# Kernel tuning notes

Measured on AMD Instinct MI355X. Metric: run time of the kernel, lower is better.

## Reference

```python
import jax, jax.numpy as jnp
import numpy as np

B, T, C = 4, 1024, 512      # batch, seq_len, n_attn
H, TT, D = 1, 1024, 16      # n_head (forced to 1 by kv.view), ctx_len, head_size


def setup_inputs() -> dict:
    key = jax.random.key(0)
    ks = jax.random.split(key, 13)
    s = 0.02
    return {
        "x": jax.random.normal(ks[0], (B, T, C), jnp.float32),
        "time_w": 1.0 + 0.1 * jax.random.normal(ks[1], (H, TT), jnp.float32),
        "time_alpha": 1.0 + 0.1 * jax.random.normal(ks[2], (H, 1, TT), jnp.float32),
        "time_beta": 1.0 + 0.1 * jax.random.normal(ks[3], (H, TT, 1), jnp.float32),
        "time_gamma": 1.0 + 0.1 * jax.random.normal(ks[4], (TT, 1), jnp.float32),
        "Wk": s * jax.random.normal(ks[5], (D, C), jnp.float32),
        "bk": jnp.zeros((D,), jnp.float32),
        "Wv": s * jax.random.normal(ks[6], (D, C), jnp.float32),
        "bv": jnp.zeros((D,), jnp.float32),
        "Wr": s * jax.random.normal(ks[7], (D, C), jnp.float32),
        "br": jnp.zeros((D,), jnp.float32),
        "Wo": s * jax.random.normal(ks[8], (64, D), jnp.float32),
        "bo": jnp.zeros((64,), jnp.float32),
    }


def reference(x, time_w, time_alpha, time_beta, time_gamma,
              Wk, bk, Wv, bv, Wr, br, Wo, bo):
    Tq = x.shape[1]
    # --- Toeplitz decay-matrix build (pad / tile / reshape trick) ---
    w = jnp.pad(time_w, ((0, 0), (0, TT)))                    # [H, 2TT]
    w = jnp.tile(w, (1, TT))[:, :-TT]                         # [H, 2TT*TT - TT]
    w = w.reshape(-1, TT, 2 * TT - 1)[:, :, TT - 1:]          # [H, TT, TT]
    w = w[:, :Tq, :Tq] * time_alpha[:, :, :Tq] * time_beta[:, :Tq, :]  # [H, T, T]
    # --- time shift on first half of channels (ZeroPad2d((0,0,1,-1))) ---
    half = x.shape[-1] // 2
    xs = jnp.pad(x[:, :, :half], ((0, 0), (1, 0), (0, 0)))[:, :-1]   # shift right by 1
    xx = jnp.concatenate([xs, x[:, :, half:]], axis=-1)              # [B, T, C]
    # --- k / v / r projections ---
    k = jnp.exp(jnp.clip(xx @ Wk.T + bk, -60.0, 30.0))        # [B, T, D]
    v = xx @ Wv.T + bv                                        # [B, T, D]
    r = xx @ Wr.T + br                                        # [B, T, D]
    sum_k = jnp.cumsum(k, axis=1)                             # [B, T, D]
    kv = k * v                                                # [B, T, D]
    # torch: kv.view(B,T,1,D).transpose(1,2) -> [B,1,T,D]; einsum 'htu,bthd->bhud'
    # broadcasts w's h=1 against kv's time axis and kv's t=1 against w's t axis:
    #   wkv[b,h,u,d] = (sum_t w[0,t,u]) * kv[b,h(time),d]
    w_sum = jnp.sum(w, axis=1)[0]                             # [T] over u
    wkv_full = w_sum[None, None, :, None] * kv[:, :, None, :] # [B, T, T, D]
    wkv = jnp.mean(wkv_full, axis=1)                          # mean over h -> [B, T, D]
    rwkv = r * wkv / (sum_k + 1e-8)                           # [B, T, D]
    out = (rwkv @ Wo.T + bo) * time_gamma[:Tq, :]             # [B, T, 64]
    return out
```

## Files before the change

kernel.cpp:

```cpp
#include <hip/hip_runtime.h>
#include <hip/hip_bf16.h>

typedef __hip_bfloat16 bf16;


__device__ __forceinline__ float ldf(const void* p, int f, long idx) {
    if (f == 0) return ((const float*)p)[idx];
    if (f == 1) {
        unsigned int u = ((unsigned int)((const unsigned short*)p)[idx]) << 16;
        float r; __builtin_memcpy(&r, &u, 4); return r;
    }
    return 0.f;
}

__global__ __launch_bounds__(64) void sniff_kernel(
    const void* p0, const void* p1, const void* p2, const void* p3,
    const void* p4, const void* p5, const void* p6, const void* p7,
    const void* p8, const void* p9, const void* p10, const void* p11,
    const void* p12,
    int n0, int n1, int n2, int n3, int n4, int n5, int n6, int n7,
    int n8, int n9, int n10, int n11, int n12,
    int* flags)
{
    const void* ps[13] = {p0,p1,p2,p3,p4,p5,p6,p7,p8,p9,p10,p11,p12};
    int ns[13] = {n0,n1,n2,n3,n4,n5,n6,n7,n8,n9,n10,n11,n12};
    int i = threadIdx.x;
    if (i < 13) {
        const unsigned short* u = (const unsigned short*)ps[i];
        int n16 = ns[i] < 64 ? ns[i] : 64;
        bool allzero = true;
        for (int j = 0; j < n16; ++j) if (u[j] != 0) { allzero = false; break; }
        int flag;
        if (allzero) flag = 2;
        else {
            int npair = n16 / 2;
            bool all_bf = true;
            for (int j = 0; j < npair; ++j) {
                unsigned short lo = u[2 * j], hi = u[2 * j + 1];
                int elo = (lo >> 7) & 0xFF, ehi = (hi >> 7) & 0xFF;
                bool lo_ok = (elo >= 64 && elo <= 190) || lo == 0;
                bool hi_ok = (ehi >= 64 && ehi <= 190) || hi == 0;
                if (!(lo_ok && hi_ok)) { all_bf = false; break; }
            }
            flag = all_bf ? 1 : 0;
        }
        flags[i] = flag;
    }
    __syncthreads();
    if (i == 0) {
        int any16 = 0;
        for (int j = 0; j < 13; ++j) if (flags[j] == 1) any16 = 1;
        flags[13] = any16;
    }
}

__global__ __launch_bounds__(256) void prep_kernel(
    const void* Wk, const void* bk, const void* Wv, const void* bv,
    const void* Wr, const void* br, const void* Wo, const void* bo,
    const void* gamma, const int* __restrict__ flg,
    float* __restrict__ WT4, float* __restrict__ biasWS,
    float* __restrict__ WoF, float* __restrict__ boF, float* __restrict__ gammaF)
{
    int idx = blockIdx.x * 256 + threadIdx.x;
    if (idx < 32768) {
        int q = idx >> 8, rem = idx & 255;
        int o = rem >> 2, c = q * 4 + (rem & 3);
        float val = 0.f;
        if (o < 16)      val = ldf(Wk, flg[5], (long)o * 512 + c);
        else if (o < 32) val = ldf(Wv, flg[7], (long)(o - 16) * 512 + c);
        else if (o < 48) val = ldf(Wr, flg[9], (long)(o - 32) * 512 + c);
        WT4[idx] = val;
    } else if (idx < 33792) {
        int i = idx - 32768;
        WoF[i] = ldf(Wo, flg[11], i);
    } else if (idx < 34816) {
        int i = idx - 33792;
        gammaF[i] = ldf(gamma, flg[4], i);
    } else if (idx < 34880) {
        int i = idx - 34816;
        boF[i] = ldf(bo, flg[12], i);
    } else if (idx < 34944) {
        int i = idx - 34880;
        float bb = 0.f;
        if (i < 16)      bb = ldf(bk, flg[6], i);
        else if (i < 32) bb = ldf(bv, flg[8], i - 16);
        else if (i < 48) bb = ldf(br, flg[10], i - 32);
        biasWS[i] = bb;
    }
}

__global__ __launch_bounds__(256) void proj_kernel(
    const void* __restrict__ x, const float* __restrict__ WT4,
    const float* __restrict__ biasWS, const int* __restrict__ flg,
    float* __restrict__ k_ws, float* __restrict__ v_ws, float* __restrict__ r_ws)
{
    __shared__ float xs[16 * 512];
    __shared__ float red[4 * 16 * 64];
    int tid = threadIdx.x;
    int row0 = blockIdx.x * 16;
    int b = row0 >> 10;
    int lt0 = row0 & 1023;
    int fx = flg[0];

    if (fx == 1) {
        const unsigned short* xp = (const unsigned short*)x;
        #pragma unroll
        for (int j = 0; j < 8; ++j) {
            int v = tid + 256 * j;
            int el = v * 4;
            int r = el >> 9, c = el & 511;
            int lt = lt0 + r - ((c < 256) ? 1 : 0);
            float4 f;
            if (lt < 0) f = make_float4(0.f, 0.f, 0.f, 0.f);
            else {
                const unsigned short* sp = xp + ((long)(b * 1024 + lt) * 512 + c);
                unsigned int u0 = ((unsigned int)sp[0]) << 16;
                unsigned int u1 = ((unsigned int)sp[1]) << 16;
                unsigned int u2 = ((unsigned int)sp[2]) << 16;
                unsigned int u3 = ((unsigned int)sp[3]) << 16;
                __builtin_memcpy(&f.x, &u0, 4); __builtin_memcpy(&f.y, &u1, 4);
                __builtin_memcpy(&f.z, &u2, 4); __builtin_memcpy(&f.w, &u3, 4);
            }
            reinterpret_cast<float4*>(xs)[v] = f;
        }
    } else {
        const float* xp = (const float*)x;
        #pragma unroll
        for (int j = 0; j < 8; ++j) {
            int v = tid + 256 * j;
            int el = v * 4;
            int r = el >> 9, c = el & 511;
            int lt = lt0 + r - ((c < 256) ? 1 : 0);
            float4 f;
            if (lt < 0) f = make_float4(0.f, 0.f, 0.f, 0.f);
            else f = *reinterpret_cast<const float4*>(xp + ((long)(b * 1024 + lt) * 512 + c));
            reinterpret_cast<float4*>(xs)[v] = f;
        }
    }
    __syncthreads();

    int o = tid & 63, cc = tid >> 6;
    const float4* xs4 = reinterpret_cast<const float4*>(xs);
    const float4* W4 = reinterpret_cast<const float4*>(WT4);
    float acc[16];
    #pragma unroll
    for (int r = 0; r < 16; ++r) acc[r] = 0.f;
    int qbase = cc * 32;
    for (int q = 0; q < 32; ++q) {
        int cq = qbase + q;
        float4 w4 = W4[cq * 64 + o];
        #pragma unroll
        for (int r = 0; r < 16; ++r) {
            float4 x4 = xs4[r * 128 + cq];
            acc[r] += x4.x * w4.x + x4.y * w4.y + x4.z * w4.z + x4.w * w4.w;
        }
    }
    #pragma unroll
    for (int r = 0; r < 16; ++r)
        red[(cc * 16 + r) * 64 + o] = acc[r];
    __syncthreads();

    #pragma unroll
    for (int it = 0; it < 4; ++it) {
        int idx = tid + 256 * it;
        int o2 = idx & 63, r2 = idx >> 6;
        float s = red[(0 * 16 + r2) * 64 + o2] + red[(1 * 16 + r2) * 64 + o2]
                + red[(2 * 16 + r2) * 64 + o2] + red[(3 * 16 + r2) * 64 + o2]
                + biasWS[o2];
        if (o2 < 48) {
            int d = o2 & 15;
            long a = (long)(lt0 + r2) * 64 + b * 16 + d;
            if (o2 < 16)      k_ws[a] = expf(fminf(fmaxf(s, -60.f), 30.f));
            else if (o2 < 32) v_ws[a] = s;
            else              r_ws[a] = s;
        }
    }
}

__global__ __launch_bounds__(64) void wsum_kernel(
    const void* __restrict__ tw, const void* __restrict__ alpha,
    const void* __restrict__ beta, const int* __restrict__ flg,
    float* __restrict__ w_sum)
{
    int ftw = flg[1], fal = flg[2], fbe = flg[3];
    int u = blockIdx.x;
    int lane = threadIdx.x;
    __shared__ float red[64];
    float acc = 0.f;
    int n = 1024 - u;
    for (int s = lane; s < n; s += 64)
        acc += ldf(tw, ftw, 1023 - s) * ldf(beta, fbe, u + s);
    red[lane] = acc;
    __syncthreads();
    for (int off = 32; off > 0; off >>= 1) {
        if (lane < off) red[lane] += red[lane + off];
        __syncthreads();
    }
    if (lane == 0) w_sum[u] = red[0] * ldf(alpha, fal, u);
}

__global__ __launch_bounds__(64) void scanA_kernel(
    const float* __restrict__ k_ws, const float* __restrict__ v_ws,
    float* __restrict__ segsum, float* __restrict__ segkv)
{
    int seg = blockIdx.x, bd = threadIdx.x;
    float part = 0.f, kvp = 0.f;
    for (int i = 0; i < 64; ++i) {
        long a = (long)(seg * 64 + i) * 64 + bd;
        float kk = k_ws[a];
        part += kk;
        kvp += kk * v_ws[a];
    }
    segsum[seg * 64 + bd] = part;
    segkv[seg * 64 + bd] = kvp;
}

__global__ __launch_bounds__(64) void scanB_kernel(
    float* k_ws, const float* __restrict__ segsum,
    const float* __restrict__ segkv, float* __restrict__ kvmean)
{
    int seg = blockIdx.x, bd = threadIdx.x;
    float run = 0.f;
    for (int s = 0; s < seg; ++s) run += segsum[s * 64 + bd];
    for (int i = 0; i < 64; ++i) {
        long a = (long)(seg * 64 + i) * 64 + bd;
        run += k_ws[a];
        k_ws[a] = run;
    }
    if (seg == 0) {
        float kvt = 0.f;
        for (int s = 0; s < 16; ++s) kvt += segkv[s * 64 + bd];
        kvmean[bd] = kvt * (1.0f / 1024.0f);
    }
}

__global__ __launch_bounds__(256) void out_kernel(
    const float* __restrict__ r_ws, const float* __restrict__ cumk,
    const float* __restrict__ kvmean, const float* __restrict__ w_sum,
    const float* __restrict__ WoF, const float* __restrict__ boF,
    const float* __restrict__ gammaF, const int* __restrict__ flg,
    void* __restrict__ out)
{
    int tid = threadIdx.x;
    int rl = tid >> 6, o = tid & 63;
    int row = blockIdx.x * 4 + rl;
    int b = row >> 10, t = row & 1023;
    __shared__ float rw[4][16];
    if (o < 16) {
        long a = (long)t * 64 + b * 16 + o;
        rw[rl][o] = r_ws[a] * w_sum[t] * kvmean[b * 16 + o] / (cumk[a] + 1e-8f);
    }
    __syncthreads();
    float acc = boF[o];
    const float4* W4 = reinterpret_cast<const float4*>(WoF + o * 16);
    #pragma unroll
    for (int j = 0; j < 4; ++j) {
        float4 w = W4[j];
        acc += rw[rl][4 * j + 0] * w.x + rw[rl][4 * j + 1] * w.y +
               rw[rl][4 * j + 2] * w.z + rw[rl][4 * j + 3] * w.w;
    }
    float val = acc * gammaF[t];
    if (flg[13]) ((bf16*)out)[(long)row * 64 + o] = __float2bfloat16(val);
    else         ((float*)out)[(long)row * 64 + o] = val;
}

extern "C" void kernel_launch(void* const* d_in, const int* in_sizes, int n_in,
                              void* d_out, int out_size, void* d_ws, size_t ws_size,
                              hipStream_t stream) {
    const void* x     = d_in[0];
    const void* tw    = d_in[1];
    const void* alpha = d_in[2];
    const void* beta  = d_in[3];
    const void* gamma = d_in[4];
    const void* Wk    = d_in[5];
    const void* bk    = d_in[6];
    const void* Wv    = d_in[7];
    const void* bv    = d_in[8];
    const void* Wr    = d_in[9];
    const void* br    = d_in[10];
    const void* Wo    = d_in[11];
    const void* bo    = d_in[12];

    float* ws     = (float*)d_ws;
    float* k_ws   = ws;
    float* v_ws   = ws + 65536;
    float* r_ws   = ws + 131072;
    float* WT4    = ws + 196608;
    float* biasWS = ws + 229376;
    float* WoF    = ws + 229440;
    float* boF    = ws + 230464;
    float* gammaF = ws + 230528;
    float* kvmean = ws + 231552;
    float* w_sum  = ws + 231616;
    float* segsum = ws + 232640;
    float* segkv  = ws + 233664;
    int*   flags  = (int*)(ws + 234688);

    sniff_kernel<<<1, 64, 0, stream>>>(
        x, tw, alpha, beta, gamma, Wk, bk, Wv, bv, Wr, br, Wo, bo,
        in_sizes[0], in_sizes[1], in_sizes[2], in_sizes[3], in_sizes[4],
        in_sizes[5], in_sizes[6], in_sizes[7], in_sizes[8], in_sizes[9],
        in_sizes[10], in_sizes[11], in_sizes[12],
        flags);
    prep_kernel<<<137, 256, 0, stream>>>(Wk, bk, Wv, bv, Wr, br, Wo, bo,
                                         gamma, flags,
                                         WT4, biasWS, WoF, boF, gammaF);
    proj_kernel<<<256, 256, 0, stream>>>(x, WT4, biasWS, flags,
                                         k_ws, v_ws, r_ws);
    wsum_kernel<<<1024, 64, 0, stream>>>(tw, alpha, beta, flags, w_sum);
    scanA_kernel<<<16, 64, 0, stream>>>(k_ws, v_ws, segsum, segkv);
    scanB_kernel<<<16, 64, 0, stream>>>(k_ws, segsum, segkv, kvmean);
    out_kernel<<<1024, 256, 0, stream>>>(r_ws, k_ws, kvmean, w_sum,
                                         WoF, boF, gammaF, flags, (void*)d_out);
}
```

Before: 123.6 us.

## Fuse sniff, prep and wsum kernels; retile projection to 8 rows per block

Merges the dtype-sniff, weight-prep and w_sum reduction kernels into one 1024-block setup kernel. Each block redoes the sniff locally into shared memory instead of relying on a separate launch, which removes two kernel launches and their serialization. The projection kernel now handles 8 rows per block over 512 blocks. Each thread computes 4 outputs across a 16-way channel split, so the kernel gets more parallelism and better register reuse of x. The cost is a larger 16-way shared-memory reduction and redundant sniff reads in every setup block.

Result: faster. 114.3 us (-7.5%).

```diff
diff --git a/kernel.cpp b/kernel.cpp
--- a/kernel.cpp
+++ b/kernel.cpp
@@ -13,80 +13,89 @@
     return 0.f;
 }
 
-__global__ __launch_bounds__(64) void sniff_kernel(
-    const void* p0, const void* p1, const void* p2, const void* p3,
-    const void* p4, const void* p5, const void* p6, const void* p7,
-    const void* p8, const void* p9, const void* p10, const void* p11,
-    const void* p12,
+__device__ __forceinline__ int sniff_one(const unsigned short* u, int els) {
+    int n16 = els < 64 ? els : 64;
+    bool allzero = true;
+    for (int j = 0; j < n16; ++j) if (u[j] != 0) { allzero = false; break; }
+    if (allzero) return 2;
+    int npair = n16 / 2;
+    for (int j = 0; j < npair; ++j) {
+        unsigned short lo = u[2 * j], hi = u[2 * j + 1];
+        int elo = (lo >> 7) & 0xFF, ehi = (hi >> 7) & 0xFF;
+        bool lo_ok = (elo >= 64 && elo <= 190) || lo == 0;
+        bool hi_ok = (ehi >= 64 && ehi <= 190) || hi == 0;
+        if (!(lo_ok && hi_ok)) return 0;
+    }
+    return 1;
+}
+
+__global__ __launch_bounds__(256) void setup_kernel(
+    const void* x, const void* tw, const void* alpha, const void* beta,
+    const void* gamma, const void* Wk, const void* bk, const void* Wv,
+    const void* bv, const void* Wr, const void* br, const void* Wo,
+    const void* bo,
     int n0, int n1, int n2, int n3, int n4, int n5, int n6, int n7,
     int n8, int n9, int n10, int n11, int n12,
-    int* flags)
-{
-    const void* ps[13] = {p0,p1,p2,p3,p4,p5,p6,p7,p8,p9,p10,p11,p12};
+    int* __restrict__ flags,
+    float* __restrict__ WT4, float* __restrict__ biasWS,
+    float* __restrict__ WoF, float* __restrict__ boF,
+    float* __restrict__ gammaF, float* __restrict__ w_sum)
+{
+    __shared__ int sf[16];
+    __shared__ float red[256];
+    int tid = threadIdx.x;
+    const void* ps[13] = {x,tw,alpha,beta,gamma,Wk,bk,Wv,bv,Wr,br,Wo,bo};
     int ns[13] = {n0,n1,n2,n3,n4,n5,n6,n7,n8,n9,n10,n11,n12};
-    int i = threadIdx.x;
-    if (i < 13) {
-        const unsigned short* u = (const unsigned short*)ps[i];
-        int n16 = ns[i] < 64 ? ns[i] : 64;
-        bool allzero = true;
-        for (int j = 0; j < n16; ++j) if (u[j] != 0) { allzero = false; break; }
-        int flag;
-        if (allzero) flag = 2;
-        else {
-            int npair = n16 / 2;
-            bool all_bf = true;
-            for (int j = 0; j < npair; ++j) {
-                unsigned short lo = u[2 * j], hi = u[2 * j + 1];
-                int elo = (lo >> 7) & 0xFF, ehi = (hi >> 7) & 0xFF;
-                bool lo_ok = (elo >= 64 && elo <= 190) || lo == 0;
-                bool hi_ok = (ehi >= 64 && ehi <= 190) || hi == 0;
-                if (!(lo_ok && hi_ok)) { all_bf = false; break; }
-            }
-            flag = all_bf ? 1 : 0;
-        }
-        flags[i] = flag;
-    }
-    __syncthreads();
-    if (i == 0) {
+    if (tid < 13) sf[tid] = sniff_one((const unsigned short*)ps[tid], ns[tid]);
+    __syncthreads();
+    if (tid == 0) {
         int any16 = 0;
-        for (int j = 0; j < 13; ++j) if (flags[j] == 1) any16 = 1;
-        flags[13] = any16;
-    }
-}
-
-__global__ __launch_bounds__(256) void prep_kernel(
-    const void* Wk, const void* bk, const void* Wv, const void* bv,
-    const void* Wr, const void* br, const void* Wo, const void* bo,
-    const void* gamma, const int* __restrict__ flg,
-    float* __restrict__ WT4, float* __restrict__ biasWS,
-    float* __restrict__ WoF, float* __restrict__ boF, float* __restrict__ gammaF)
-{
-    int idx = blockIdx.x * 256 + threadIdx.x;
+        for (int j = 0; j < 13; ++j) if (sf[j] == 1) any16 = 1;
+        sf[13] = any16;
+    }
+    __syncthreads();
+    if (blockIdx.x == 0 && tid < 14) flags[tid] = sf[tid];
+
+    int idx = blockIdx.x * 256 + tid;
     if (idx < 32768) {
         int q = idx >> 8, rem = idx & 255;
         int o = rem >> 2, c = q * 4 + (rem & 3);
         float val = 0.f;
-        if (o < 16)      val = ldf(Wk, flg[5], (long)o * 512 + c);
-        else if (o < 32) val = ldf(Wv, flg[7], (long)(o - 16) * 512 + c);
-        else if (o < 48) val = ldf(Wr, flg[9], (long)(o - 32) * 512 + c);
+        if (o < 16)      val = ldf(Wk, sf[5], (long)o * 512 + c);
+        else if (o < 32) val = ldf(Wv, sf[7], (long)(o - 16) * 512 + c);
+        else if (o < 48) val = ldf(Wr, sf[9], (long)(o - 32) * 512 + c);
         WT4[idx] = val;
     } else if (idx < 33792) {
         int i = idx - 32768;
-        WoF[i] = ldf(Wo, flg[11], i);
+        WoF[i] = ldf(Wo, sf[11], i);
     } else if (idx < 34816) {
         int i = idx - 33792;
-        gammaF[i] = ldf(gamma, flg[4], i);
+        gammaF[i] = ldf(gamma, sf[4], i);
     } else if (idx < 34880) {
         int i = idx - 34816;
-        boF[i] = ldf(bo, flg[12], i);
+        boF[i] = ldf(bo, sf[12], i);
     } else if (idx < 34944) {
         int i = idx - 34880;
         float bb = 0.f;
-        if (i < 16)      bb = ldf(bk, flg[6], i);
-        else if (i < 32) bb = ldf(bv, flg[8], i - 16);
-        else if (i < 48) bb = ldf(br, flg[10], i - 32);
+        if (i < 16)      bb = ldf(bk, sf[6], i);
+        else if (i < 32) bb = ldf(bv, sf[8], i - 16);
+        else if (i < 48) bb = ldf(br, sf[10], i - 32);
         biasWS[i] = bb;
     }
+
+    int u = blockIdx.x;
+    int ftw = sf[1], fal = sf[2], fbe = sf[3];
+    float acc = 0.f;
+    int n = 1024 - u;
+    for (int s = tid; s < n; s += 256)
+        acc += ldf(tw, ftw, 1023 - s) * ldf(beta, fbe, u + s);
+    red[tid] = acc;
+    __syncthreads();
+    for (int off = 128; off > 0; off >>= 1) {
+        if (tid < off) red[tid] += red[tid + off];
+        __syncthreads();
+    }
+    if (tid == 0) w_sum[u] = red[0] * ldf(alpha, fal, u);
 }
 
 __global__ __launch_bounds__(256) void proj_kernel(
@@ -94,10 +103,10 @@
     const float* __restrict__ biasWS, const int* __restrict__ flg,
     float* __restrict__ k_ws, float* __restrict__ v_ws, float* __restrict__ r_ws)
 {
-    __shared__ float xs[16 * 512];
-    __shared__ float red[4 * 16 * 64];
+    __shared__ float xs[8 * 512];
+    __shared__ float red[16 * 8 * 64];
     int tid = threadIdx.x;
-    int row0 = blockIdx.x * 16;
+    int row0 = blockIdx.x * 8;
     int b = row0 >> 10;
     int lt0 = row0 & 1023;
     int fx = flg[0];
@@ -105,7 +114,7 @@
     if (fx == 1) {
         const unsigned short* xp = (const unsigned short*)x;
         #pragma unroll
-        for (int j = 0; j < 8; ++j) {
+        for (int j = 0; j < 4; ++j) {
             int v = tid + 256 * j;
             int el = v * 4;
             int r = el >> 9, c = el & 511;
@@ -126,7 +135,7 @@
     } else {
         const float* xp = (const float*)x;
         #pragma unroll
-        for (int j = 0; j < 8; ++j) {
+        for (int j = 0; j < 4; ++j) {
             int v = tid + 256 * j;
             int el = v * 4;
             int r = el >> 9, c = el & 511;
@@ -139,34 +148,42 @@
     }
     __syncthreads();
 
-    int o = tid & 63, cc = tid >> 6;
+    int o4 = tid & 15, cc = tid >> 4;
     const float4* xs4 = reinterpret_cast<const float4*>(xs);
     const float4* W4 = reinterpret_cast<const float4*>(WT4);
-    float acc[16];
-    #pragma unroll
-    for (int r = 0; r < 16; ++r) acc[r] = 0.f;
-    int qbase = cc * 32;
-    for (int q = 0; q < 32; ++q) {
-        int cq = qbase + q;
-        float4 w4 = W4[cq * 64 + o];
+    float a0[8], a1[8], a2[8], a3[8];
+    #pragma unroll
+    for (int r = 0; r < 8; ++r) { a0[r] = a1[r] = a2[r] = a3[r] = 0.f; }
+    #pragma unroll
+    for (int q = 0; q < 8; ++q) {
+        int cq = cc * 8 + q;
+        float4 w0 = W4[cq * 64 + o4 * 4 + 0];
+        float4 w1 = W4[cq * 64 + o4 * 4 + 1];
+        float4 w2 = W4[cq * 64 + o4 * 4 + 2];
+        float4 w3 = W4[cq * 64 + o4 * 4 + 3];
         #pragma unroll
-        for (int r = 0; r < 16; ++r) {
+        for (int r = 0; r < 8; ++r) {
             float4 x4 = xs4[r * 128 + cq];
-            acc[r] += x4.x * w4.x + x4.y * w4.y + x4.z * w4.z + x4.w * w4.w;
+            a0[r] += x4.x * w0.x + x4.y * w0.y + x4.z * w0.z + x4.w * w0.w;
+            a1[r] += x4.x * w1.x + x4.y * w1.y + x4.z * w1.z + x4.w * w1.w;
+            a2[r] += x4.x * w2.x + x4.y * w2.y + x4.z * w2.z + x4.w * w2.w;
+            a3[r] += x4.x * w3.x + x4.y * w3.y + x4.z * w3.z + x4.w * w3.w;
         }
     }
-    #pragma unroll
-    for (int r = 0; r < 16; ++r)
-        red[(cc * 16 + r) * 64 + o] = acc[r];
-    __syncthreads();
-
-    #pragma unroll
-    for (int it = 0; it < 4; ++it) {
+    float4* red4 = reinterpret_cast<float4*>(red);
+    #pragma unroll
+    for (int r = 0; r < 8; ++r)
+        red4[(cc * 8 + r) * 16 + o4] = make_float4(a0[r], a1[r], a2[r], a3[r]);
+    __syncthreads();
+
+    #pragma unroll
+    for (int it = 0; it < 2; ++it) {
         int idx = tid + 256 * it;
         int o2 = idx & 63, r2 = idx >> 6;
-        float s = red[(0 * 16 + r2) * 64 + o2] + red[(1 * 16 + r2) * 64 + o2]
-                + red[(2 * 16 + r2) * 64 + o2] + red[(3 * 16 + r2) * 64 + o2]
-                + biasWS[o2];
+        float s = biasWS[o2];
+        #pragma unroll
+        for (int cc2 = 0; cc2 < 16; ++cc2)
+            s += red[(cc2 * 8 + r2) * 64 + o2];
         if (o2 < 48) {
             int d = o2 & 15;
             long a = (long)(lt0 + r2) * 64 + b * 16 + d;
@@ -175,28 +192,6 @@
             else              r_ws[a] = s;
         }
     }
-}
-
-__global__ __launch_bounds__(64) void wsum_kernel(
-    const void* __restrict__ tw, const void* __restrict__ alpha,
-    const void* __restrict__ beta, const int* __restrict__ flg,
-    float* __restrict__ w_sum)
-{
-    int ftw = flg[1], fal = flg[2], fbe = flg[3];
-    int u = blockIdx.x;
-    int lane = threadIdx.x;
-    __shared__ float red[64];
-    float acc = 0.f;
-    int n = 1024 - u;
-    for (int s = lane; s < n; s += 64)
-        acc += ldf(tw, ftw, 1023 - s) * ldf(beta, fbe, u + s);
-    red[lane] = acc;
-    __syncthreads();
-    for (int off = 32; off > 0; off >>= 1) {
-        if (lane < off) red[lane] += red[lane + off];
-        __syncthreads();
-    }
-    if (lane == 0) w_sum[u] = red[0] * ldf(alpha, fal, u);
 }
 
 __global__ __launch_bounds__(64) void scanA_kernel(
@@ -296,18 +291,14 @@
     float* segkv  = ws + 233664;
     int*   flags  = (int*)(ws + 234688);
 
-    sniff_kernel<<<1, 64, 0, stream>>>(
+    setup_kernel<<<1024, 256, 0, stream>>>(
         x, tw, alpha, beta, gamma, Wk, bk, Wv, bv, Wr, br, Wo, bo,
         in_sizes[0], in_sizes[1], in_sizes[2], in_sizes[3], in_sizes[4],
         in_sizes[5], in_sizes[6], in_sizes[7], in_sizes[8], in_sizes[9],
         in_sizes[10], in_sizes[11], in_sizes[12],
-        flags);
-    prep_kernel<<<137, 256, 0, stream>>>(Wk, bk, Wv, bv, Wr, br, Wo, bo,
-                                         gamma, flags,
-                                         WT4, biasWS, WoF, boF, gammaF);
-    proj_kernel<<<256, 256, 0, stream>>>(x, WT4, biasWS, flags,
+        flags, WT4, biasWS, WoF, boF, gammaF, w_sum);
+    proj_kernel<<<512, 256, 0, stream>>>(x, WT4, biasWS, flags,
                                          k_ws, v_ws, r_ws);
-    wsum_kernel<<<1024, 64, 0, stream>>>(tw, alpha, beta, flags, w_sum);
     scanA_kernel<<<16, 64, 0, stream>>>(k_ws, v_ws, segsum, segkv);
     scanB_kernel<<<16, 64, 0, stream>>>(k_ws, segsum, segkv, kvmean);
     out_kernel<<<1024, 256, 0, stream>>>(r_ws, k_ws, kvmean, w_sum,
```
